# Kernel tuning notes

Measured on AMD Instinct MI355X. Metric: run time of the kernel, lower is better.

Reference implementation:

```python
import math
import jax, jax.numpy as jnp
import numpy as np

# ---- static module config ----
DIM = 256
NUM_HEADS = 8
WS = (12, 12)            # window size
L = WS[0] * WS[1]        # window area = 144
META_HIDDEN = 384
LOGIT_MAX = math.log(1.0 / 0.01)  # clamp max for logit scale


def _relative_coords_log() -> np.ndarray:
    """Log-spaced pairwise relative coordinates, shape (L*L, 2)."""
    ys, xs = np.meshgrid(np.arange(WS[0]), np.arange(WS[1]), indexing="ij")
    coords = np.stack([ys.ravel(), xs.ravel()], axis=0)          # (2, L)
    rel = coords[:, :, None] - coords[:, None, :]                # (2, L, L)
    rel = rel.transpose(1, 2, 0).reshape(-1, 2).astype(np.float32)
    return np.sign(rel) * np.log1p(np.abs(rel))

REL_COORDS_LOG = jnp.asarray(_relative_coords_log())  # (L*L, 2)


def setup_inputs() -> dict:
    key = jax.random.key(0)
    ks = jax.random.split(key, 12)
    Bw, C, H = 1024, DIM, NUM_HEADS
    num_win = 64
    inp = {
        "x": jax.random.normal(ks[0], (Bw, L, C), dtype=jnp.float32),
        "mask": jax.random.normal(ks[1], (num_win, L, L), dtype=jnp.float32),
        # qkv / proj linears
        "qkv_w": jax.random.normal(ks[2], (3 * C, C), dtype=jnp.float32) * (1.0 / math.sqrt(C)),
        "qkv_b": jnp.zeros((3 * C,), dtype=jnp.float32),
        "proj_w": jax.random.normal(ks[3], (C, C), dtype=jnp.float32) * (1.0 / math.sqrt(C)),
        "proj_b": jnp.zeros((C,), dtype=jnp.float32),
        # meta MLP: 2 -> META_HIDDEN -> H
        "fc1_w": jax.random.normal(ks[4], (META_HIDDEN, 2), dtype=jnp.float32) * 0.5,
        "fc1_b": jnp.zeros((META_HIDDEN,), dtype=jnp.float32),
        "fc2_w": jax.random.normal(ks[5], (H, META_HIDDEN), dtype=jnp.float32) * (1.0 / math.sqrt(META_HIDDEN)),
        "fc2_b": jnp.zeros((H,), dtype=jnp.float32),
        # learnable per-head logit scale, init log(10)
        "logit_scale": jnp.full((H,), math.log(10.0), dtype=jnp.float32),
    }
    return inp


def reference(x, mask, qkv_w, qkv_b, proj_w, proj_b, fc1_w, fc1_b, fc2_w, fc2_b, logit_scale):
    Bw, Lx, C = x.shape
    H = NUM_HEADS
    Dh = C // H

    # qkv projection -> (3, Bw, H, L, Dh)
    qkv = (x @ qkv_w.T + qkv_b).reshape(Bw, Lx, 3, H, Dh).transpose(2, 0, 3, 1, 4)
    q, k, v = qkv[0], qkv[1], qkv[2]

    # cosine attention: L2-normalize q and k (eps as in F.normalize)
    qn = q / jnp.maximum(jnp.linalg.norm(q, axis=-1, keepdims=True), 1e-12)
    kn = k / jnp.maximum(jnp.linalg.norm(k, axis=-1, keepdims=True), 1e-12)
    attn = jnp.einsum("bhld,bhmd->bhlm", qn, kn)  # (Bw, H, L, L)

    # clamped learnable logit scale
    scale = jnp.exp(jnp.minimum(logit_scale, LOGIT_MAX)).reshape(1, H, 1, 1)
    attn = attn * scale

    # continuous relative position bias via meta MLP (L*L, 2) -> (L*L, H)
    hbias = jax.nn.relu(REL_COORDS_LOG @ fc1_w.T + fc1_b) @ fc2_w.T + fc2_b
    rel_bias = hbias.T.reshape(1, H, Lx, Lx)
    attn = attn + rel_bias

    # shift mask: (num_win, L, L) broadcast over batch and heads
    num_win = mask.shape[0]
    attn = attn.reshape(Bw // num_win, num_win, H, Lx, Lx) + mask[None, :, None, :, :]
    attn = attn.reshape(Bw, H, Lx, Lx)

    attn = jax.nn.softmax(attn, axis=-1)

    out = jnp.einsum("bhlm,bhmd->bhld", attn, v)  # (Bw, H, L, Dh)
    out = out.transpose(0, 2, 1, 3).reshape(Bw, Lx, C)
    out = out @ proj_w.T + proj_b
    return out
```

## Files before the change

### kernel.cpp

```cpp
#include <hip/hip_runtime.h>
#include <stdint.h>


typedef __attribute__((ext_vector_type(4))) float floatx4;
typedef __attribute__((ext_vector_type(8))) __bf16 bf16x8;

#define LOGIT_MAX 4.6051701859880914f

__device__ __forceinline__ uint16_t f2bf(float f) {
    union { float f32; uint32_t u; } x;
    x.f32 = f;
    uint32_t r = x.u + 0x7FFFu + ((x.u >> 16) & 1u);
    return (uint16_t)(r >> 16);
}

__device__ __forceinline__ bf16x8 cvt8(const float* __restrict__ p) {
    const floatx4 a = *(const floatx4*)p;
    const floatx4 b = *(const floatx4*)(p + 4);
    union { bf16x8 v; uint16_t u[8]; } r;
    r.u[0] = f2bf(a[0]); r.u[1] = f2bf(a[1]); r.u[2] = f2bf(a[2]); r.u[3] = f2bf(a[3]);
    r.u[4] = f2bf(b[0]); r.u[5] = f2bf(b[1]); r.u[6] = f2bf(b[2]); r.u[7] = f2bf(b[3]);
    return r.v;
}

__device__ __forceinline__ void glds16(const uint16_t* g, uint16_t* l) {
    __builtin_amdgcn_global_load_lds((const __attribute__((address_space(1))) uint32_t*)g,
                                     (__attribute__((address_space(3))) uint32_t*)l, 16, 0, 0);
}

__global__ __launch_bounds__(256) void cvtw_kernel(const float* __restrict__ qkvw,
                                                   const float* __restrict__ projw,
                                                   uint16_t* __restrict__ wqkv,
                                                   uint16_t* __restrict__ wproj) {
    const int i = blockIdx.x * 256 + threadIdx.x;
    if (i < 768 * 256) wqkv[i] = f2bf(qkvw[i]);
    if (i < 256 * 256) wproj[i] = f2bf(projw[i]);
}

__global__ __launch_bounds__(256) void rbias_kernel(const float* __restrict__ fc1w,
                                                    const float* __restrict__ fc1b,
                                                    const float* __restrict__ fc2w,
                                                    const float* __restrict__ fc2b,
                                                    float* __restrict__ outb) {
    __shared__ float w1a[384], w1b[384], b1[384];
    __shared__ float w2[8 * 384];
    for (int i = threadIdx.x; i < 384; i += 256) {
        w1a[i] = fc1w[2 * i];
        w1b[i] = fc1w[2 * i + 1];
        b1[i]  = fc1b[i];
    }
    for (int i = threadIdx.x; i < 3072; i += 256) w2[i] = fc2w[i];
    __syncthreads();
    const int p = blockIdx.x * 256 + threadIdx.x;
    if (p >= 144 * 144) return;
    const int i = p / 144;
    const int j = p - i * 144;
    const float dy = (float)(i / 12 - j / 12);
    const float dx = (float)(i % 12 - j % 12);
    const float cy = (dy > 0.f ? 1.f : (dy < 0.f ? -1.f : 0.f)) * log1pf(fabsf(dy));
    const float cx = (dx > 0.f ? 1.f : (dx < 0.f ? -1.f : 0.f)) * log1pf(fabsf(dx));
    float acc[8] = {0, 0, 0, 0, 0, 0, 0, 0};
    for (int t = 0; t < 384; t++) {
        float hv = fmaf(cy, w1a[t], fmaf(cx, w1b[t], b1[t]));
        hv = fmaxf(hv, 0.f);
#pragma unroll
        for (int hh = 0; hh < 8; hh++) acc[hh] = fmaf(hv, w2[hh * 384 + t], acc[hh]);
    }
#pragma unroll
    for (int hh = 0; hh < 8; hh++) outb[(size_t)hh * 20736 + p] = acc[hh] + fc2b[hh];
}

__global__ __launch_bounds__(256) void gemm_qkv_kernel(const float* __restrict__ x,
                                                       const uint16_t* __restrict__ W,
                                                       const float* __restrict__ bias,
                                                       uint16_t* __restrict__ outq) {
    __shared__ __align__(16) uint16_t sA[8192];
    __shared__ __align__(16) uint16_t sB[8192];
    const int tid  = threadIdx.x;
    const int lane = tid & 63;
    const int w    = tid >> 6;
    const int wr   = (w >> 1) << 6;
    const int wc   = (w & 1) << 6;
    const int lr   = lane & 15;
    const int q4   = lane >> 4;
    const int brow = (blockIdx.x / 6) << 7;
    const int bcol = (blockIdx.x % 6) << 7;

    floatx4 acc[4][4];
#pragma unroll
    for (int m = 0; m < 4; m++)
#pragma unroll
        for (int n = 0; n < 4; n++) acc[m][n] = (floatx4){0.f, 0.f, 0.f, 0.f};

#pragma unroll 1
    for (int ks = 0; ks < 4; ++ks) {
        const int bk = ks << 6;
        __syncthreads();
#pragma unroll
        for (int i = 0; i < 4; ++i) {
            const int c = (i << 8) + tid;
            const int r = c >> 3, s = c & 7;
            const int sg = s ^ (r & 7);
            const bf16x8 v = cvt8(x + (size_t)(brow + r) * 256 + bk + (sg << 3));
            *(bf16x8*)&sA[c << 3] = v;
        }
#pragma unroll
        for (int i = 0; i < 4; ++i) {
            const int c = (i << 8) + tid;
            const int r = c >> 3, s = c & 7;
            const int sg = s ^ (r & 7);
            glds16(W + (size_t)(bcol + r) * 256 + bk + (sg << 3),
                   &sB[(size_t)((i << 8) + (w << 6)) << 3]);
        }
        __syncthreads();
#pragma unroll
        for (int kk = 0; kk < 2; ++kk) {
            const int cb = (kk << 6) + (q4 << 4);
            bf16x8 af[4], bfq[4];
#pragma unroll
            for (int m = 0; m < 4; ++m) {
                const int r = wr + (m << 4) + lr;
                af[m] = *(const bf16x8*)((const char*)sA + r * 128 + (cb ^ ((r & 7) << 4)));
            }
#pragma unroll
            for (int n = 0; n < 4; ++n) {
                const int r = wc + (n << 4) + lr;
                bfq[n] = *(const bf16x8*)((const char*)sB + r * 128 + (cb ^ ((r & 7) << 4)));
            }
#pragma unroll
            for (int m = 0; m < 4; ++m)
#pragma unroll
                for (int n = 0; n < 4; ++n)
                    acc[m][n] = __builtin_amdgcn_mfma_f32_16x16x32_bf16(af[m], bfq[n], acc[m][n], 0, 0, 0);
        }
    }
#pragma unroll
    for (int n = 0; n < 4; ++n) {
        const float bb = bias[bcol + wc + (n << 4) + lr];
#pragma unroll
        for (int m = 0; m < 4; ++m)
#pragma unroll
            for (int r = 0; r < 4; ++r) acc[m][n][r] += bb;
    }
    if (bcol < 512) {
#pragma unroll
        for (int m = 0; m < 4; ++m)
#pragma unroll
            for (int np = 0; np < 4; np += 2)
#pragma unroll
                for (int r = 0; r < 4; ++r) {
                    float ss = acc[m][np][r] * acc[m][np][r] + acc[m][np + 1][r] * acc[m][np + 1][r];
#pragma unroll
                    for (int o = 1; o < 16; o <<= 1) ss += __shfl_xor(ss, o, 64);
                    const float rn = 1.0f / fmaxf(sqrtf(ss), 1e-12f);
                    acc[m][np][r] *= rn;
                    acc[m][np + 1][r] *= rn;
                }
    }
#pragma unroll
    for (int m = 0; m < 4; ++m)
#pragma unroll
        for (int r = 0; r < 4; ++r) {
            const size_t row = (size_t)(brow + wr + (m << 4) + (q4 << 2) + r);
#pragma unroll
            for (int n = 0; n < 4; ++n)
                outq[row * 768 + bcol + wc + (n << 4) + lr] = f2bf(acc[m][n][r]);
        }
}

__global__ __launch_bounds__(576, 2) void attn_kernel(const uint16_t* __restrict__ qkv,
                                                      const float* __restrict__ mask,
                                                      const float* __restrict__ rbias,
                                                      const float* __restrict__ lsc,
                                                      uint16_t* __restrict__ ob,
                                                      const int win_base) {
    __shared__ __align__(16) uint16_t sm[29568];
    uint16_t* const PB = sm;
    uint16_t* const qn = sm;
    uint16_t* const kn = sm + 5760;
    uint16_t* const vT = sm + 24192;

    const int wl   = blockIdx.x >> 3;
    const int h    = blockIdx.x & 7;
    const int tid  = threadIdx.x;
    const int lane = tid & 63;
    const int mi   = tid >> 6;
    const int lr   = lane & 15;
    const int kq   = (lane >> 4) << 3;
    const int rq   = (lane >> 4) << 2;
    const int arow = mi * 16 + lr;

    {
        const int l  = tid >> 2;
        const int d0 = (tid & 3) << 3;
        const uint16_t* base = qkv + (size_t)(wl * 144 + l) * 768 + h * 32 + d0;
        *(bf16x8*)&qn[l * 40 + d0] = *(const bf16x8*)(base);
        *(bf16x8*)&kn[l * 40 + d0] = *(const bf16x8*)(base + 256);
        union { bf16x8 v; uint16_t u[8]; } vv;
        vv.v = *(const bf16x8*)(base + 512);
#pragma unroll
        for (int u = 0; u < 8; ++u) vT[(d0 + u) * 168 + l] = vv.u[u];
        for (int i = tid; i < 32 * 24; i += 576) vT[(i / 24) * 168 + 144 + (i % 24)] = 0;
    }
    __syncthreads();

    const float scale = __expf(fminf(lsc[h], LOGIT_MAX));
    const float* bh = rbias + (size_t)h * 20736;
    const float* mw = mask + (size_t)((win_base + wl) & 63) * 20736;
    const bf16x8 aq = *(const bf16x8*)&qn[arow * 40 + kq];
    float sl[9][4];
#pragma unroll
    for (int ni = 0; ni < 9; ni++) {
        const bf16x8 bkf = *(const bf16x8*)&kn[(ni * 16 + lr) * 40 + kq];
        floatx4 s = (floatx4){0.f, 0.f, 0.f, 0.f};
        s = __builtin_amdgcn_mfma_f32_16x16x32_bf16(aq, bkf, s, 0, 0, 0);
#pragma unroll
        for (int r = 0; r < 4; r++) {
            const int row = mi * 16 + rq + r;
            const int col = ni * 16 + lr;
            sl[ni][r] = s[r] * scale + bh[row * 144 + col] + mw[row * 144 + col];
        }
    }
#pragma unroll
    for (int r = 0; r < 4; r++) {
        float m = -3.0e38f;
#pragma unroll
        for (int ni = 0; ni < 9; ni++) m = fmaxf(m, sl[ni][r]);
#pragma unroll
        for (int o = 1; o < 16; o <<= 1) m = fmaxf(m, __shfl_xor(m, o, 64));
        float s = 0.f;
#pragma unroll
        for (int ni = 0; ni < 9; ni++) {
            float e = __expf(sl[ni][r] - m);
            sl[ni][r] = e;
            s += e;
        }
#pragma unroll
        for (int o = 1; o < 16; o <<= 1) s += __shfl_xor(s, o, 64);
        const float inv = 1.0f / s;
#pragma unroll
        for (int ni = 0; ni < 9; ni++) sl[ni][r] *= inv;
    }
    __syncthreads();

#pragma unroll
    for (int ni = 0; ni < 9; ni++)
#pragma unroll
        for (int r = 0; r < 4; r++)
            PB[(mi * 16 + rq + r) * 168 + ni * 16 + lr] = f2bf(sl[ni][r]);
#pragma unroll
    for (int u = 0; u < 6; ++u) {
        const int idx = u * 64 + lane;
        PB[(mi * 16 + (idx / 24)) * 168 + 144 + (idx % 24)] = 0;
    }
    __syncthreads();

    floatx4 o0 = (floatx4){0.f, 0.f, 0.f, 0.f};
    floatx4 o1 = (floatx4){0.f, 0.f, 0.f, 0.f};
#pragma unroll
    for (int kt = 0; kt < 5; kt++) {
        const bf16x8 pa = *(const bf16x8*)&PB[arow * 168 + kt * 32 + kq];
        const bf16x8 v0 = *(const bf16x8*)&vT[lr * 168 + kt * 32 + kq];
        const bf16x8 v1 = *(const bf16x8*)&vT[(16 + lr) * 168 + kt * 32 + kq];
        o0 = __builtin_amdgcn_mfma_f32_16x16x32_bf16(pa, v0, o0, 0, 0, 0);
        o1 = __builtin_amdgcn_mfma_f32_16x16x32_bf16(pa, v1, o1, 0, 0, 0);
    }
#pragma unroll
    for (int r = 0; r < 4; r++) {
        const size_t row = (size_t)wl * 144 + mi * 16 + rq + r;
        ob[row * 256 + h * 32 + lr]      = f2bf(o0[r]);
        ob[row * 256 + h * 32 + 16 + lr] = f2bf(o1[r]);
    }
}

__global__ __launch_bounds__(256) void gemm_proj_kernel(const uint16_t* __restrict__ A,
                                                        const uint16_t* __restrict__ W,
                                                        const float* __restrict__ bias,
                                                        float* __restrict__ outp) {
    __shared__ __align__(16) uint16_t sA[8192];
    __shared__ __align__(16) uint16_t sB[8192];
    const int tid  = threadIdx.x;
    const int lane = tid & 63;
    const int w    = tid >> 6;
    const int wr   = (w >> 1) << 6;
    const int wc   = (w & 1) << 6;
    const int lr   = lane & 15;
    const int q4   = lane >> 4;
    const int brow = (blockIdx.x >> 1) << 7;
    const int bcol = (blockIdx.x & 1) << 7;

    floatx4 acc[4][4];
#pragma unroll
    for (int m = 0; m < 4; m++)
#pragma unroll
        for (int n = 0; n < 4; n++) acc[m][n] = (floatx4){0.f, 0.f, 0.f, 0.f};

#pragma unroll 1
    for (int ks = 0; ks < 4; ++ks) {
        const int bk = ks << 6;
        __syncthreads();
#pragma unroll
        for (int i = 0; i < 4; ++i) {
            const int c = (i << 8) + tid;
            const int r = c >> 3, s = c & 7;
            const int sg = s ^ (r & 7);
            glds16(A + (size_t)(brow + r) * 256 + bk + (sg << 3),
                   &sA[(size_t)((i << 8) + (w << 6)) << 3]);
        }
#pragma unroll
        for (int i = 0; i < 4; ++i) {
            const int c = (i << 8) + tid;
            const int r = c >> 3, s = c & 7;
            const int sg = s ^ (r & 7);
            glds16(W + (size_t)(bcol + r) * 256 + bk + (sg << 3),
                   &sB[(size_t)((i << 8) + (w << 6)) << 3]);
        }
        __syncthreads();
#pragma unroll
        for (int kk = 0; kk < 2; ++kk) {
            const int cb = (kk << 6) + (q4 << 4);
            bf16x8 af[4], bfq[4];
#pragma unroll
            for (int m = 0; m < 4; ++m) {
                const int r = wr + (m << 4) + lr;
                af[m] = *(const bf16x8*)((const char*)sA + r * 128 + (cb ^ ((r & 7) << 4)));
            }
#pragma unroll
            for (int n = 0; n < 4; ++n) {
                const int r = wc + (n << 4) + lr;
                bfq[n] = *(const bf16x8*)((const char*)sB + r * 128 + (cb ^ ((r & 7) << 4)));
            }
#pragma unroll
            for (int m = 0; m < 4; ++m)
#pragma unroll
                for (int n = 0; n < 4; ++n)
                    acc[m][n] = __builtin_amdgcn_mfma_f32_16x16x32_bf16(af[m], bfq[n], acc[m][n], 0, 0, 0);
        }
    }
#pragma unroll
    for (int n = 0; n < 4; ++n) {
        const float bb = bias[bcol + wc + (n << 4) + lr];
#pragma unroll
        for (int m = 0; m < 4; ++m)
#pragma unroll
            for (int r = 0; r < 4; ++r) {
                const size_t row = (size_t)(brow + wr + (m << 4) + (q4 << 2) + r);
                outp[row * 256 + bcol + wc + (n << 4) + lr] = acc[m][n][r] + bb;
            }
    }
}

extern "C" void kernel_launch(void* const* d_in, const int* in_sizes, int n_in,
                              void* d_out, int out_size, void* d_ws, size_t ws_size,
                              hipStream_t stream) {
    (void)in_sizes; (void)n_in; (void)out_size;
    const float* x      = (const float*)d_in[0];
    const float* mask   = (const float*)d_in[1];
    const float* qkv_w  = (const float*)d_in[2];
    const float* qkv_b  = (const float*)d_in[3];
    const float* proj_w = (const float*)d_in[4];
    const float* proj_b = (const float*)d_in[5];
    const float* fc1_w  = (const float*)d_in[6];
    const float* fc1_b  = (const float*)d_in[7];
    const float* fc2_w  = (const float*)d_in[8];
    const float* fc2_b  = (const float*)d_in[9];
    const float* lsc    = (const float*)d_in[10];
    float* out = (float*)d_out;

    float* bias_ws  = (float*)d_ws;
    uint16_t* wqkv  = (uint16_t*)(bias_ws + 165888);
    uint16_t* wproj = wqkv + 196608;
    uint16_t* dyn   = wproj + 65536;

    int CH = 1;
    while (CH < 128) {
        const size_t need = 1187840ULL + ((size_t)(1024 / CH) * 144) * 2048ULL;
        if (need <= ws_size) break;
        CH <<= 1;
    }
    const int WPC = 1024 / CH;
    const int MC  = WPC * 144;
    uint16_t* qkvws = dyn;
    uint16_t* obws  = dyn + (size_t)MC * 768;

    cvtw_kernel<<<768, 256, 0, stream>>>(qkv_w, proj_w, wqkv, wproj);
    rbias_kernel<<<81, 256, 0, stream>>>(fc1_w, fc1_b, fc2_w, fc2_b, bias_ws);
    for (int c = 0; c < CH; ++c) {
        const float* xc = x + (size_t)c * MC * 256;
        gemm_qkv_kernel<<<(MC / 128) * 6, 256, 0, stream>>>(xc, wqkv, qkv_b, qkvws);
        attn_kernel<<<WPC * 8, 576, 0, stream>>>(qkvws, mask, bias_ws, lsc, obws, c * WPC);
        gemm_proj_kernel<<<(MC / 128) * 2, 256, 0, stream>>>(obws, wproj, proj_b,
                                                             out + (size_t)c * MC * 256);
    }
}
```

Baseline: 763.6 us.

## Make attention persistent with prefetch, pre-convert x to bf16, swizzle blocks across XCDs

Attention now launches 64×8 blocks. Each block loops over windows that share the same mask index, prefetching the next window's q/k/v into registers while it computes the current one, so the mask and bias tiles stay warm in cache. A separate kernel converts x to bf16 once, and the QKV GEMM then loads A with direct global-to-LDS copies instead of converting fp32 in every column block. All kernels remap block IDs so neighbouring tiles land on the same XCD. The softmax folds log2e into the scale to use exp2, and the V transpose writes are rotated to reduce LDS bank conflicts. In exchange this adds an extra pass that writes and re-reads bf16 x, more workspace, and fewer concurrent blocks for attention.

```diff
diff --git a/kernel.cpp b/kernel.cpp
--- a/kernel.cpp
+++ b/kernel.cpp
@@ -6,6 +6,7 @@
 typedef __attribute__((ext_vector_type(8))) __bf16 bf16x8;
 
 #define LOGIT_MAX 4.6051701859880914f
+#define LOG2E 1.4426950408889634f
 
 __device__ __forceinline__ uint16_t f2bf(float f) {
     union { float f32; uint32_t u; } x;
@@ -35,6 +36,12 @@
     const int i = blockIdx.x * 256 + threadIdx.x;
     if (i < 768 * 256) wqkv[i] = f2bf(qkvw[i]);
     if (i < 256 * 256) wproj[i] = f2bf(projw[i]);
+}
+
+__global__ __launch_bounds__(256) void cvtx_kernel(const float* __restrict__ x,
+                                                   uint16_t* __restrict__ xb) {
+    const size_t i = (size_t)blockIdx.x * 256 + threadIdx.x;
+    *(bf16x8*)(xb + i * 8) = cvt8(x + i * 8);
 }
 
 __global__ __launch_bounds__(256) void rbias_kernel(const float* __restrict__ fc1w,
@@ -70,7 +77,7 @@
     for (int hh = 0; hh < 8; hh++) outb[(size_t)hh * 20736 + p] = acc[hh] + fc2b[hh];
 }
 
-__global__ __launch_bounds__(256) void gemm_qkv_kernel(const float* __restrict__ x,
+__global__ __launch_bounds__(256) void gemm_qkv_kernel(const uint16_t* __restrict__ xb,
                                                        const uint16_t* __restrict__ W,
                                                        const float* __restrict__ bias,
                                                        uint16_t* __restrict__ outq) {
@@ -83,8 +90,13 @@
     const int wc   = (w & 1) << 6;
     const int lr   = lane & 15;
     const int q4   = lane >> 4;
-    const int brow = (blockIdx.x / 6) << 7;
-    const int bcol = (blockIdx.x % 6) << 7;
+    int bid = blockIdx.x;
+    if ((gridDim.x & 7) == 0) {
+        const int per = gridDim.x >> 3;
+        bid = (bid & 7) * per + (bid >> 3);
+    }
+    const int brow = (bid / 6) << 7;
+    const int bcol = (bid % 6) << 7;
 
     floatx4 acc[4][4];
 #pragma unroll
@@ -101,8 +113,8 @@
             const int c = (i << 8) + tid;
             const int r = c >> 3, s = c & 7;
             const int sg = s ^ (r & 7);
-            const bf16x8 v = cvt8(x + (size_t)(brow + r) * 256 + bk + (sg << 3));
-            *(bf16x8*)&sA[c << 3] = v;
+            glds16(xb + (size_t)(brow + r) * 256 + bk + (sg << 3),
+                   &sA[(size_t)((i << 8) + (w << 6)) << 3]);
         }
 #pragma unroll
         for (int i = 0; i < 4; ++i) {
@@ -173,15 +185,20 @@
                                                       const float* __restrict__ rbias,
                                                       const float* __restrict__ lsc,
                                                       uint16_t* __restrict__ ob,
-                                                      const int win_base) {
+                                                      const int win_base, const int G) {
     __shared__ __align__(16) uint16_t sm[29568];
     uint16_t* const PB = sm;
     uint16_t* const qn = sm;
     uint16_t* const kn = sm + 5760;
     uint16_t* const vT = sm + 24192;
 
-    const int wl   = blockIdx.x >> 3;
-    const int h    = blockIdx.x & 7;
+    int bid = blockIdx.x;
+    if ((gridDim.x & 7) == 0) {
+        const int per = gridDim.x >> 3;
+        bid = (bid & 7) * per + (bid >> 3);
+    }
+    const int s4   = bid >> 3;
+    const int h    = bid & 7;
     const int tid  = threadIdx.x;
     const int lane = tid & 63;
     const int mi   = tid >> 6;
@@ -190,86 +207,108 @@
     const int rq   = (lane >> 4) << 2;
     const int arow = mi * 16 + lr;
 
-    {
-        const int l  = tid >> 2;
-        const int d0 = (tid & 3) << 3;
-        const uint16_t* base = qkv + (size_t)(wl * 144 + l) * 768 + h * 32 + d0;
-        *(bf16x8*)&qn[l * 40 + d0] = *(const bf16x8*)(base);
-        *(bf16x8*)&kn[l * 40 + d0] = *(const bf16x8*)(base + 256);
-        union { bf16x8 v; uint16_t u[8]; } vv;
-        vv.v = *(const bf16x8*)(base + 512);
-#pragma unroll
-        for (int u = 0; u < 8; ++u) vT[(d0 + u) * 168 + l] = vv.u[u];
-        for (int i = tid; i < 32 * 24; i += 576) vT[(i / 24) * 168 + 144 + (i % 24)] = 0;
-    }
-    __syncthreads();
-
-    const float scale = __expf(fminf(lsc[h], LOGIT_MAX));
+    const float scale2 = __expf(fminf(lsc[h], LOGIT_MAX)) * LOG2E;
     const float* bh = rbias + (size_t)h * 20736;
-    const float* mw = mask + (size_t)((win_base + wl) & 63) * 20736;
-    const bf16x8 aq = *(const bf16x8*)&qn[arow * 40 + kq];
-    float sl[9][4];
-#pragma unroll
-    for (int ni = 0; ni < 9; ni++) {
-        const bf16x8 bkf = *(const bf16x8*)&kn[(ni * 16 + lr) * 40 + kq];
-        floatx4 s = (floatx4){0.f, 0.f, 0.f, 0.f};
-        s = __builtin_amdgcn_mfma_f32_16x16x32_bf16(aq, bkf, s, 0, 0, 0);
+    const float* mw = mask + (size_t)((win_base + s4) & 63) * 20736;
+
+    const int l   = tid >> 2;
+    const int d0  = (tid & 3) << 3;
+    const int rot = d0 >> 3;
+
+    for (int i = tid; i < 32 * 24; i += 576) vT[(i / 24) * 168 + 144 + (i % 24)] = 0;
+
+    const uint16_t* base0 = qkv + ((size_t)s4 * 144 + l) * 768 + h * 32 + d0;
+    bf16x8 pq = *(const bf16x8*)(base0);
+    bf16x8 pk = *(const bf16x8*)(base0 + 256);
+    bf16x8 pv = *(const bf16x8*)(base0 + 512);
+
+#pragma unroll 1
+    for (int t = 0; t < G; ++t) {
+        *(bf16x8*)&qn[l * 40 + d0] = pq;
+        *(bf16x8*)&kn[l * 40 + d0] = pk;
+        {
+            union { bf16x8 v; uint16_t u[8]; } vv;
+            vv.v = pv;
+#pragma unroll
+            for (int u = 0; u < 8; ++u) {
+                const int rr = (u + rot) & 7;
+                vT[(d0 + rr) * 168 + l] = vv.u[rr];
+            }
+        }
+        __syncthreads();
+
+        if (t + 1 < G) {
+            const uint16_t* base = qkv + ((size_t)(s4 + ((t + 1) << 6)) * 144 + l) * 768 + h * 32 + d0;
+            pq = *(const bf16x8*)(base);
+            pk = *(const bf16x8*)(base + 256);
+            pv = *(const bf16x8*)(base + 512);
+        }
+
+        const bf16x8 aq = *(const bf16x8*)&qn[arow * 40 + kq];
+        float sl[9][4];
+#pragma unroll
+        for (int ni = 0; ni < 9; ni++) {
+            const bf16x8 bkf = *(const bf16x8*)&kn[(ni * 16 + lr) * 40 + kq];
+            floatx4 s = (floatx4){0.f, 0.f, 0.f, 0.f};
+            s = __builtin_amdgcn_mfma_f32_16x16x32_bf16(aq, bkf, s, 0, 0, 0);
+#pragma unroll
+            for (int r = 0; r < 4; r++) {
+                const int row = mi * 16 + rq + r;
+                const int col = ni * 16 + lr;
+                sl[ni][r] = fmaf(s[r], scale2, (bh[row * 144 + col] + mw[row * 144 + col]) * LOG2E);
+            }
+        }
 #pragma unroll
         for (int r = 0; r < 4; r++) {
-            const int row = mi * 16 + rq + r;
-            const int col = ni * 16 + lr;
-            sl[ni][r] = s[r] * scale + bh[row * 144 + col] + mw[row * 144 + col];
-        }
-    }
-#pragma unroll
-    for (int r = 0; r < 4; r++) {
-        float m = -3.0e38f;
-#pragma unroll
-        for (int ni = 0; ni < 9; ni++) m = fmaxf(m, sl[ni][r]);
-#pragma unroll
-        for (int o = 1; o < 16; o <<= 1) m = fmaxf(m, __shfl_xor(m, o, 64));
-        float s = 0.f;
-#pragma unroll
-        for (int ni = 0; ni < 9; ni++) {
-            float e = __expf(sl[ni][r] - m);
-            sl[ni][r] = e;
-            s += e;
-        }
-#pragma unroll
-        for (int o = 1; o < 16; o <<= 1) s += __shfl_xor(s, o, 64);
-        const float inv = 1.0f / s;
-#pragma unroll
-        for (int ni = 0; ni < 9; ni++) sl[ni][r] *= inv;
-    }
-    __syncthreads();
-
-#pragma unroll
-    for (int ni = 0; ni < 9; ni++)
-#pragma unroll
-        for (int r = 0; r < 4; r++)
-            PB[(mi * 16 + rq + r) * 168 + ni * 16 + lr] = f2bf(sl[ni][r]);
-#pragma unroll
-    for (int u = 0; u < 6; ++u) {
-        const int idx = u * 64 + lane;
-        PB[(mi * 16 + (idx / 24)) * 168 + 144 + (idx % 24)] = 0;
-    }
-    __syncthreads();
-
-    floatx4 o0 = (floatx4){0.f, 0.f, 0.f, 0.f};
-    floatx4 o1 = (floatx4){0.f, 0.f, 0.f, 0.f};
-#pragma unroll
-    for (int kt = 0; kt < 5; kt++) {
-        const bf16x8 pa = *(const bf16x8*)&PB[arow * 168 + kt * 32 + kq];
-        const bf16x8 v0 = *(const bf16x8*)&vT[lr * 168 + kt * 32 + kq];
-        const bf16x8 v1 = *(const bf16x8*)&vT[(16 + lr) * 168 + kt * 32 + kq];
-        o0 = __builtin_amdgcn_mfma_f32_16x16x32_bf16(pa, v0, o0, 0, 0, 0);
-        o1 = __builtin_amdgcn_mfma_f32_16x16x32_bf16(pa, v1, o1, 0, 0, 0);
-    }
-#pragma unroll
-    for (int r = 0; r < 4; r++) {
-        const size_t row = (size_t)wl * 144 + mi * 16 + rq + r;
-        ob[row * 256 + h * 32 + lr]      = f2bf(o0[r]);
-        ob[row * 256 + h * 32 + 16 + lr] = f2bf(o1[r]);
+            float m = -3.0e38f;
+#pragma unroll
+            for (int ni = 0; ni < 9; ni++) m = fmaxf(m, sl[ni][r]);
+#pragma unroll
+            for (int o = 1; o < 16; o <<= 1) m = fmaxf(m, __shfl_xor(m, o, 64));
+            float s = 0.f;
+#pragma unroll
+            for (int ni = 0; ni < 9; ni++) {
+                float e = exp2f(sl[ni][r] - m);
+                sl[ni][r] = e;
+                s += e;
+            }
+#pragma unroll
+            for (int o = 1; o < 16; o <<= 1) s += __shfl_xor(s, o, 64);
+            const float inv = 1.0f / s;
+#pragma unroll
+            for (int ni = 0; ni < 9; ni++) sl[ni][r] *= inv;
+        }
+        __syncthreads();
+
+#pragma unroll
+        for (int ni = 0; ni < 9; ni++)
+#pragma unroll
+            for (int r = 0; r < 4; r++)
+                PB[(mi * 16 + rq + r) * 168 + ni * 16 + lr] = f2bf(sl[ni][r]);
+#pragma unroll
+        for (int u = 0; u < 6; ++u) {
+            const int idx = u * 64 + lane;
+            PB[(mi * 16 + (idx / 24)) * 168 + 144 + (idx % 24)] = 0;
+        }
+        __syncthreads();
+
+        floatx4 o0 = (floatx4){0.f, 0.f, 0.f, 0.f};
+        floatx4 o1 = (floatx4){0.f, 0.f, 0.f, 0.f};
+#pragma unroll
+        for (int kt = 0; kt < 5; kt++) {
+            const bf16x8 pa = *(const bf16x8*)&PB[arow * 168 + kt * 32 + kq];
+            const bf16x8 v0 = *(const bf16x8*)&vT[lr * 168 + kt * 32 + kq];
+            const bf16x8 v1 = *(const bf16x8*)&vT[(16 + lr) * 168 + kt * 32 + kq];
+            o0 = __builtin_amdgcn_mfma_f32_16x16x32_bf16(pa, v0, o0, 0, 0, 0);
+            o1 = __builtin_amdgcn_mfma_f32_16x16x32_bf16(pa, v1, o1, 0, 0, 0);
+        }
+#pragma unroll
+        for (int r = 0; r < 4; r++) {
+            const size_t row = ((size_t)s4 + ((size_t)t << 6)) * 144 + mi * 16 + rq + r;
+            ob[row * 256 + h * 32 + lr]      = f2bf(o0[r]);
+            ob[row * 256 + h * 32 + 16 + lr] = f2bf(o1[r]);
+        }
+        __syncthreads();
     }
 }
 
@@ -286,8 +325,13 @@
     const int wc   = (w & 1) << 6;
     const int lr   = lane & 15;
     const int q4   = lane >> 4;
-    const int brow = (blockIdx.x >> 1) << 7;
-    const int bcol = (blockIdx.x & 1) << 7;
+    int bid = blockIdx.x;
+    if ((gridDim.x & 7) == 0) {
+        const int per = gridDim.x >> 3;
+        bid = (bid & 7) * per + (bid >> 3);
+    }
+    const int brow = (bid >> 1) << 7;
+    const int bcol = (bid & 1) << 7;
 
     floatx4 acc[4][4];
 #pragma unroll
@@ -374,21 +418,26 @@
 
     int CH = 1;
     while (CH < 128) {
-        const size_t need = 1187840ULL + ((size_t)(1024 / CH) * 144) * 2048ULL;
+        const size_t need = 1187840ULL + ((size_t)(1024 / CH) * 144) * 2560ULL;
         if (need <= ws_size) break;
         CH <<= 1;
     }
     const int WPC = 1024 / CH;
     const int MC  = WPC * 144;
-    uint16_t* qkvws = dyn;
-    uint16_t* obws  = dyn + (size_t)MC * 768;
+    uint16_t* xbws  = dyn;
+    uint16_t* qkvws = xbws + (size_t)MC * 256;
+    uint16_t* obws  = qkvws + (size_t)MC * 768;
+
+    const int S_att = (WPC >= 64) ? 64 : WPC;
+    const int G     = WPC / S_att;
 
     cvtw_kernel<<<768, 256, 0, stream>>>(qkv_w, proj_w, wqkv, wproj);
     rbias_kernel<<<81, 256, 0, stream>>>(fc1_w, fc1_b, fc2_w, fc2_b, bias_ws);
     for (int c = 0; c < CH; ++c) {
-        const float* xc = x + (size_t)c * MC * 256;
-        gemm_qkv_kernel<<<(MC / 128) * 6, 256, 0, stream>>>(xc, wqkv, qkv_b, qkvws);
-        attn_kernel<<<WPC * 8, 576, 0, stream>>>(qkvws, mask, bias_ws, lsc, obws, c * WPC);
+        cvtx_kernel<<<MC / 8, 256, 0, stream>>>(x + (size_t)c * MC * 256, xbws);
+        gemm_qkv_kernel<<<(MC / 128) * 6, 256, 0, stream>>>(xbws, wqkv, qkv_b, qkvws);
+        attn_kernel<<<S_att * 8, 576, 0, stream>>>(qkvws, mask, bias_ws, lsc, obws,
+                                                   c * WPC, G);
         gemm_proj_kernel<<<(MC / 128) * 2, 256, 0, stream>>>(obws, wproj, proj_b,
                                                              out + (size_t)c * MC * 256);
     }
```

Measured after the change: 704.4 us. 1.08x faster.
